# Kernel optimization log

Measured on AMD Instinct MI355X. Metric: run time of the kernel, lower is better.

## Reference

```python
import jax, jax.numpy as jnp
import numpy as np

N_NODES = 50000
N_EDGES = 800000
IN_DIM = 64
HID = 64
NUM_GRAPHS = 512


def _gcn_conv(x, W, b, row, col, norm, n):
    # PyG GCNConv: h = x @ W; out[col] += norm * h[row]; out += b
    h = x @ W  # [N, HID]
    msg = h[row] * norm[:, None]  # [E', HID]
    out = jax.ops.segment_sum(msg, col, num_segments=n)
    return out + b


def setup_inputs() -> dict:
    key = jax.random.key(0)
    ks = jax.random.split(key, 12)
    x = jax.random.normal(ks[0], (N_NODES, IN_DIM), dtype=jnp.float32)
    edge_index = jax.random.randint(ks[1], (2, N_EDGES), 0, N_NODES, dtype=jnp.int64)
    batch = jnp.sort(jax.random.randint(ks[2], (N_NODES,), 0, NUM_GRAPHS, dtype=jnp.int64))
    s = 0.05
    W1 = jax.random.normal(ks[3], (IN_DIM, HID), dtype=jnp.float32) * s
    b1 = jnp.zeros((HID,), dtype=jnp.float32)
    W2 = jax.random.normal(ks[4], (HID, HID), dtype=jnp.float32) * s
    b2 = jnp.zeros((HID,), dtype=jnp.float32)
    W3 = jax.random.normal(ks[5], (HID, HID), dtype=jnp.float32) * s
    b3 = jnp.zeros((HID,), dtype=jnp.float32)
    lin_W = jax.random.normal(ks[6], (HID, 1), dtype=jnp.float32) * s
    lin_b = jnp.zeros((1,), dtype=jnp.float32)
    return {"x": x, "W1": W1, "b1": b1, "W2": W2, "b2": b2, "W3": W3,
            "b3": b3, "lin_W": lin_W, "lin_b": lin_b,
            "edge_index": edge_index, "batch": batch}


def reference(x, W1, b1, W2, b2, W3, b3, lin_W, lin_b, edge_index, batch):
    n = x.shape[0]
    # add self-loops (GCNConv default add_self_loops=True)
    loop = jnp.arange(n, dtype=edge_index.dtype)
    row = jnp.concatenate([edge_index[0], loop])  # source
    col = jnp.concatenate([edge_index[1], loop])  # target (aggregation index)
    # symmetric degree normalization: deg over targets with unit weights
    deg = jax.ops.segment_sum(jnp.ones_like(col, dtype=x.dtype), col, num_segments=n)
    dinv = jnp.where(deg > 0, jax.lax.rsqrt(deg), 0.0)
    norm = dinv[row] * dinv[col]  # [E+N]

    h = jax.nn.relu(_gcn_conv(x, W1, b1, row, col, norm, n))
    h = jax.nn.relu(_gcn_conv(h, W2, b2, row, col, norm, n))
    h = _gcn_conv(h, W3, b3, row, col, norm, n)

    # global_mean_pool over batch ids
    sums = jax.ops.segment_sum(h, batch, num_segments=NUM_GRAPHS)
    cnt = jax.ops.segment_sum(jnp.ones((n,), dtype=h.dtype), batch, num_segments=NUM_GRAPHS)
    pooled = sums / jnp.maximum(cnt, 1.0)[:, None]
    # dropout p=0.5 is identity in eval mode
    return pooled @ lin_W + lin_b  # [NUM_GRAPHS, 1]
```

## Files before the change

### kernel.cpp

```cpp
#include <hip/hip_runtime.h>
#include <hip/hip_fp16.h>

#define NN 50000
#define NE 800000
#define HD 64
#define NG 512
#define NBK 196
#define NBL 196
#define M_CNT (NBK * NBL)
#define NBS 151
#define GEMM_BLOCKS 3125

__global__ void zero_kernel(int* __restrict__ p, int n) {
    int i = blockIdx.x * blockDim.x + threadIdx.x;
    if (i < n) p[i] = 0;
}

__global__ __launch_bounds__(256) void bucket_count(const int* __restrict__ col,
                                                    const int* __restrict__ batch,
                                                    int* __restrict__ counts,
                                                    int* __restrict__ beg,
                                                    int* __restrict__ endx) {
    __shared__ int hist[256];
    int tid = threadIdx.x, blk = blockIdx.x;
    hist[tid] = 0;
    __syncthreads();
    int base = blk * 4096;
#pragma unroll
    for (int k = 0; k < 16; ++k) {
        int e = base + k * 256 + tid;
        if (e < NE) atomicAdd(&hist[col[e] >> 8], 1);
    }
    int t = blk * 256 + tid;
    if (t < NN) {
        int g = batch[t];
        if (t == 0 || batch[t - 1] != g) beg[g] = t;
        if (t == NN - 1 || batch[t + 1] != g) endx[g] = t + 1;
    }
    __syncthreads();
    if (tid < NBK) counts[tid * NBL + blk] = hist[tid];
}

__global__ __launch_bounds__(256) void block_reduce(const int* __restrict__ src,
                                                    int* __restrict__ bsum) {
    __shared__ int ws[4];
    int tid = threadIdx.x, lane = tid & 63, wid = tid >> 6;
    int i = blockIdx.x * 256 + tid;
    int v = (i < M_CNT) ? src[i] : 0;
#pragma unroll
    for (int off = 32; off > 0; off >>= 1) v += __shfl_down(v, off, 64);
    if (lane == 0) ws[wid] = v;
    __syncthreads();
    if (tid == 0) bsum[blockIdx.x] = ws[0] + ws[1] + ws[2] + ws[3];
}

__global__ __launch_bounds__(64) void scan_bsum(int* __restrict__ bsum) {
    int lane = threadIdx.x;
    int carry = 0;
    for (int base = 0; base < NBS; base += 64) {
        int i = base + lane;
        int v = (i < NBS) ? bsum[i] : 0;
        int inc = v;
#pragma unroll
        for (int off = 1; off < 64; off <<= 1) {
            int t = __shfl_up(inc, off, 64);
            if (lane >= off) inc += t;
        }
        if (i < NBS) bsum[i] = carry + inc - v;
        carry += __shfl(inc, 63, 64);
    }
}

__global__ __launch_bounds__(256) void block_scan(const int* __restrict__ src,
                                                  const int* __restrict__ bsum,
                                                  int* __restrict__ dst) {
    __shared__ int ws[4];
    int tid = threadIdx.x, lane = tid & 63, wid = tid >> 6;
    int i = blockIdx.x * 256 + tid;
    int v = (i < M_CNT) ? src[i] : 0;
    int inc = v;
#pragma unroll
    for (int off = 1; off < 64; off <<= 1) {
        int t = __shfl_up(inc, off, 64);
        if (lane >= off) inc += t;
    }
    if (lane == 63) ws[wid] = inc;
    __syncthreads();
    int woff = 0;
    for (int k = 0; k < wid; ++k) woff += ws[k];
    if (i < M_CNT) dst[i] = bsum[blockIdx.x] + woff + inc - v;
}

__global__ __launch_bounds__(256) void gemm1_scatter(const float* __restrict__ x,
                                                     const float* __restrict__ W1,
                                                     __half* __restrict__ h16,
                                                     const int* __restrict__ row,
                                                     const int* __restrict__ col,
                                                     const int* __restrict__ counts_ex,
                                                     unsigned* __restrict__ packed) {
    if (blockIdx.x < GEMM_BLOCKS) {
        __shared__ float Ws[64][64];
        __shared__ float Is[16][64];
        int t = threadIdx.x;
        for (int i = t; i < 64 * 64; i += 256) Ws[i >> 6][i & 63] = W1[i];
        int row0 = blockIdx.x * 16;
        for (int i = t; i < 16 * 64; i += 256)
            Is[i >> 6][i & 63] = x[(row0 + (i >> 6)) * HD + (i & 63)];
        __syncthreads();
        int c = t & 63, r4 = t >> 6;
        float a0 = 0.f, a1 = 0.f, a2 = 0.f, a3 = 0.f;
#pragma unroll
        for (int k = 0; k < 64; ++k) {
            float w = Ws[k][c];
            a0 += Is[r4 + 0][k] * w;
            a1 += Is[r4 + 4][k] * w;
            a2 += Is[r4 + 8][k] * w;
            a3 += Is[r4 + 12][k] * w;
        }
        h16[(row0 + r4 + 0) * HD + c] = __float2half(a0);
        h16[(row0 + r4 + 4) * HD + c] = __float2half(a1);
        h16[(row0 + r4 + 8) * HD + c] = __float2half(a2);
        h16[(row0 + r4 + 12) * HD + c] = __float2half(a3);
    } else {
        __shared__ int cur[256];
        int tid = threadIdx.x, blk = blockIdx.x - GEMM_BLOCKS;
        cur[tid] = 0;
        __syncthreads();
        int base = blk * 4096;
#pragma unroll
        for (int k = 0; k < 16; ++k) {
            int e = base + k * 256 + tid;
            if (e < NE) {
                int c = col[e], r = row[e];
                int b = c >> 8;
                int lpos = atomicAdd(&cur[b], 1);
                int pos = counts_ex[b * NBL + blk] + lpos;
                packed[pos] = (unsigned)r | ((unsigned)(c & 255) << 16);
            }
        }
    }
}

__global__ __launch_bounds__(256) void csr_rowptr(const unsigned* __restrict__ packed,
                                                  const int* __restrict__ counts_ex,
                                                  int* __restrict__ rowptr,
                                                  float* __restrict__ dinv) {
    __shared__ int hist[256];
    __shared__ int ws[4];
    int bkt = blockIdx.x, tid = threadIdx.x;
    int s = counts_ex[bkt * NBL];
    int e = (bkt == NBK - 1) ? NE : counts_ex[(bkt + 1) * NBL];
    hist[tid] = 0;
    __syncthreads();
    for (int j = s + tid; j < e; j += 256)
        atomicAdd(&hist[(packed[j] >> 16) & 255], 1);
    __syncthreads();
    int lane = tid & 63, wid = tid >> 6;
    int v = hist[tid], inc = v;
#pragma unroll
    for (int off = 1; off < 64; off <<= 1) {
        int t = __shfl_up(inc, off, 64);
        if (lane >= off) inc += t;
    }
    if (lane == 63) ws[wid] = inc;
    __syncthreads();
    int woff = 0;
    for (int k = 0; k < wid; ++k) woff += ws[k];
    int node = bkt * 256 + tid;
    if (node < NN) {
        rowptr[node] = s + woff + inc - v;
        dinv[node] = rsqrtf((float)(v + 1));
    }
    if (bkt == 0 && tid == 0) rowptr[NN] = NE;
}

__global__ __launch_bounds__(256) void csr_fill(const unsigned* __restrict__ packed,
                                                const int* __restrict__ counts_ex,
                                                const int* __restrict__ rowptr,
                                                const float* __restrict__ dinv,
                                                int2* __restrict__ ew) {
    __shared__ int cur[256];
    int bkt = blockIdx.x, tid = threadIdx.x;
    int s = counts_ex[bkt * NBL];
    int e = (bkt == NBK - 1) ? NE : counts_ex[(bkt + 1) * NBL];
    cur[tid] = 0;
    __syncthreads();
    for (int j = s + tid; j < e; j += 256) {
        unsigned p = packed[j];
        int r = p & 0xFFFF;
        int lc = (p >> 16) & 255;
        int c = (bkt << 8) | lc;
        int slot = rowptr[c] + atomicAdd(&cur[lc], 1);
        float w = dinv[r] * dinv[c];
        ew[slot] = make_int2(r, __float_as_int(w));
    }
}

__global__ __launch_bounds__(256) void gemm64_f16(const __half* __restrict__ in,
                                                  const float* __restrict__ W,
                                                  __half* __restrict__ out) {
    __shared__ float Ws[64][64];
    __shared__ float Is[16][64];
    int t = threadIdx.x;
    for (int i = t; i < 64 * 64; i += 256) Ws[i >> 6][i & 63] = W[i];
    int row0 = blockIdx.x * 16;
    const __half2* in2 = (const __half2*)(in + (size_t)row0 * HD);
    for (int i = t; i < 16 * 32; i += 256) {
        float2 v = __half22float2(in2[i]);
        int r = i >> 5, c2 = (i & 31) * 2;
        Is[r][c2]     = fmaxf(v.x, 0.f);
        Is[r][c2 + 1] = fmaxf(v.y, 0.f);
    }
    __syncthreads();
    int c = t & 63, r4 = t >> 6;
    float a0 = 0.f, a1 = 0.f, a2 = 0.f, a3 = 0.f;
#pragma unroll
    for (int k = 0; k < 64; ++k) {
        float w = Ws[k][c];
        a0 += Is[r4 + 0][k] * w;
        a1 += Is[r4 + 4][k] * w;
        a2 += Is[r4 + 8][k] * w;
        a3 += Is[r4 + 12][k] * w;
    }
    out[(row0 + r4 + 0) * HD + c] = __float2half(a0);
    out[(row0 + r4 + 4) * HD + c] = __float2half(a1);
    out[(row0 + r4 + 8) * HD + c] = __float2half(a2);
    out[(row0 + r4 + 12) * HD + c] = __float2half(a3);
}

template <bool POOL>
__global__ __launch_bounds__(256) void gather_h16(const __half* __restrict__ h16,
                                                  const int* __restrict__ rowptr,
                                                  const int2* __restrict__ ew,
                                                  const float* __restrict__ dinv,
                                                  const float* __restrict__ b,
                                                  __half* __restrict__ out16,
                                                  const int* __restrict__ batch,
                                                  float* __restrict__ pooled) {
    int tid = threadIdx.x, lane = tid & 63, wid = tid >> 6;
    int hh = lane >> 5, c = lane & 31;
    int node = blockIdx.x * 4 + wid;
    const __half2* hv = (const __half2*)h16;
    int s = rowptr[node], e = rowptr[node + 1];
    float2 acc;
    if (hh == 0) {
        float di = dinv[node], dd = di * di;
        float2 self = __half22float2(hv[node * 32 + c]);
        float2 bb = ((const float2*)b)[c];
        acc.x = dd * self.x + bb.x;
        acc.y = dd * self.y + bb.y;
    } else {
        acc.x = 0.f; acc.y = 0.f;
    }
    int nfull = (e - s) & ~7;
    int j = s + hh, jend = s + nfull;
    for (; j < jend; j += 8) {
        int2 p0 = ew[j], p1 = ew[j + 2], p2 = ew[j + 4], p3 = ew[j + 6];
        __half2 v0 = hv[p0.x * 32 + c];
        __half2 v1 = hv[p1.x * 32 + c];
        __half2 v2 = hv[p2.x * 32 + c];
        __half2 v3 = hv[p3.x * 32 + c];
        float w0 = __int_as_float(p0.y), w1 = __int_as_float(p1.y);
        float w2 = __int_as_float(p2.y), w3 = __int_as_float(p3.y);
        float2 f0 = __half22float2(v0), f1 = __half22float2(v1);
        float2 f2 = __half22float2(v2), f3 = __half22float2(v3);
        acc.x += w0 * f0.x + w1 * f1.x + w2 * f2.x + w3 * f3.x;
        acc.y += w0 * f0.y + w1 * f1.y + w2 * f2.y + w3 * f3.y;
    }
    for (; j < e; j += 2) {
        int2 p = ew[j];
        __half2 v = hv[p.x * 32 + c];
        float w = __int_as_float(p.y);
        float2 f = __half22float2(v);
        acc.x += w * f.x;
        acc.y += w * f.y;
    }
    acc.x += __shfl_xor(acc.x, 32, 64);
    acc.y += __shfl_xor(acc.y, 32, 64);
    if (hh == 0) {
        if (POOL) {
            int g = batch[node];
            atomicAdd(&pooled[g * HD + 2 * c], acc.x);
            atomicAdd(&pooled[g * HD + 2 * c + 1], acc.y);
        } else {
            ((__half2*)out16)[node * 32 + c] = __floats2half2_rn(acc.x, acc.y);
        }
    }
}

__global__ __launch_bounds__(64) void final_kernel(const float* __restrict__ pooled,
                                                   const int* __restrict__ beg,
                                                   const int* __restrict__ endx,
                                                   const float* __restrict__ lin_W,
                                                   const float* __restrict__ lin_b,
                                                   float* __restrict__ out) {
    int g = blockIdx.x, d = threadIdx.x;
    float cnt = (float)(endx[g] - beg[g]);
    float v = pooled[g * HD + d] / fmaxf(cnt, 1.f) * lin_W[d];
#pragma unroll
    for (int off = 32; off > 0; off >>= 1) v += __shfl_down(v, off, 64);
    if (d == 0) out[g] = v + lin_b[0];
}

extern "C" void kernel_launch(void* const* d_in, const int* in_sizes, int n_in,
                              void* d_out, int out_size, void* d_ws, size_t ws_size,
                              hipStream_t stream) {
    const float* x     = (const float*)d_in[0];
    const float* W1    = (const float*)d_in[1];
    const float* b1    = (const float*)d_in[2];
    const float* W2    = (const float*)d_in[3];
    const float* b2    = (const float*)d_in[4];
    const float* W3    = (const float*)d_in[5];
    const float* b3    = (const float*)d_in[6];
    const float* lin_W = (const float*)d_in[7];
    const float* lin_b = (const float*)d_in[8];
    const int* edge_index = (const int*)d_in[9];
    const int* batch      = (const int*)d_in[10];
    const int* row = edge_index;
    const int* col = edge_index + NE;
    float* out = (float*)d_out;

    __half*   h16       = (__half*)d_ws;
    __half*   A16       = h16 + (size_t)NN * HD;
    int2*     ew        = (int2*)(A16 + (size_t)NN * HD);
    unsigned* packed    = (unsigned*)(ew + NE);
    int*      counts    = (int*)(packed + NE);
    int*      counts_ex = counts + M_CNT;
    int*      rowptr    = counts_ex + M_CNT;
    float*    dinv      = (float*)(rowptr + NN + 2);
    int*      bsum      = (int*)(dinv + NN);
    float*    pooled    = (float*)(bsum + 256);
    int*      beg       = (int*)(pooled + NG * HD);
    int*      endx      = beg + NG;

    const int ZN = NG * HD + 2 * NG;
    zero_kernel<<<(ZN + 255) / 256, 256, 0, stream>>>((int*)pooled, ZN);

    bucket_count<<<NBL, 256, 0, stream>>>(col, batch, counts, beg, endx);
    block_reduce<<<NBS, 256, 0, stream>>>(counts, bsum);
    scan_bsum<<<1, 64, 0, stream>>>(bsum);
    block_scan<<<NBS, 256, 0, stream>>>(counts, bsum, counts_ex);
    gemm1_scatter<<<GEMM_BLOCKS + NBL, 256, 0, stream>>>(x, W1, h16, row, col,
                                                         counts_ex, packed);
    csr_rowptr<<<NBK, 256, 0, stream>>>(packed, counts_ex, rowptr, dinv);
    csr_fill<<<NBK, 256, 0, stream>>>(packed, counts_ex, rowptr, dinv, ew);

    const int GB = NN / 4;

    gather_h16<false><<<GB, 256, 0, stream>>>(h16, rowptr, ew, dinv, b1, A16,
                                              batch, pooled);
    gemm64_f16<<<GEMM_BLOCKS, 256, 0, stream>>>(A16, W2, h16);
    gather_h16<false><<<GB, 256, 0, stream>>>(h16, rowptr, ew, dinv, b2, A16,
                                              batch, pooled);
    gemm64_f16<<<GEMM_BLOCKS, 256, 0, stream>>>(A16, W3, h16);
    gather_h16<true><<<GB, 256, 0, stream>>>(h16, rowptr, ew, dinv, b3, nullptr,
                                             batch, pooled);

    final_kernel<<<NG, 64, 0, stream>>>(pooled, beg, endx, lin_W, lin_b, out);
}
```

Baseline: 283.3 us.

## Split feature matrix into two 32-column planes and gather each plane separately

Stores the fp16 hidden features as two planar halves of 32 columns each instead of row-major 64 columns. Each sparse gather pass is now run twice, once per plane, so the gathered working set per pass is half the size and more likely to stay resident in cache. Edge-list reads and output writes switch to nontemporal loads and stores, and each wavefront now covers four edges at a time with 16 lanes. The cost is reading the edge list twice per layer and launching twice as many gather kernels.

```diff
diff --git a/kernel.cpp b/kernel.cpp
--- a/kernel.cpp
+++ b/kernel.cpp
@@ -10,6 +10,7 @@
 #define M_CNT (NBK * NBL)
 #define NBS 151
 #define GEMM_BLOCKS 3125
+
 
 __global__ void zero_kernel(int* __restrict__ p, int n) {
     int i = blockIdx.x * blockDim.x + threadIdx.x;
@@ -117,10 +118,11 @@
             a2 += Is[r4 + 8][k] * w;
             a3 += Is[r4 + 12][k] * w;
         }
-        h16[(row0 + r4 + 0) * HD + c] = __float2half(a0);
-        h16[(row0 + r4 + 4) * HD + c] = __float2half(a1);
-        h16[(row0 + r4 + 8) * HD + c] = __float2half(a2);
-        h16[(row0 + r4 + 12) * HD + c] = __float2half(a3);
+        size_t pb = (size_t)(c >> 5) * NN * 32 + (c & 31);
+        h16[pb + (size_t)(row0 + r4 + 0) * 32] = __float2half(a0);
+        h16[pb + (size_t)(row0 + r4 + 4) * 32] = __float2half(a1);
+        h16[pb + (size_t)(row0 + r4 + 8) * 32] = __float2half(a2);
+        h16[pb + (size_t)(row0 + r4 + 12) * 32] = __float2half(a3);
     } else {
         __shared__ int cur[256];
         int tid = threadIdx.x, blk = blockIdx.x - GEMM_BLOCKS;
@@ -204,12 +206,17 @@
     int t = threadIdx.x;
     for (int i = t; i < 64 * 64; i += 256) Ws[i >> 6][i & 63] = W[i];
     int row0 = blockIdx.x * 16;
-    const __half2* in2 = (const __half2*)(in + (size_t)row0 * HD);
-    for (int i = t; i < 16 * 32; i += 256) {
-        float2 v = __half22float2(in2[i]);
-        int r = i >> 5, c2 = (i & 31) * 2;
-        Is[r][c2]     = fmaxf(v.x, 0.f);
-        Is[r][c2 + 1] = fmaxf(v.y, 0.f);
+    const __half2* p0 = (const __half2*)(in + (size_t)row0 * 32);
+    const __half2* p1 = (const __half2*)(in + ((size_t)NN + row0) * 32);
+    {
+        int i = t;
+        int r = i >> 4, cc = (i & 15) * 2;
+        float2 v = __half22float2(p0[i]);
+        Is[r][cc]     = fmaxf(v.x, 0.f);
+        Is[r][cc + 1] = fmaxf(v.y, 0.f);
+        float2 w = __half22float2(p1[i]);
+        Is[r][32 + cc]     = fmaxf(w.x, 0.f);
+        Is[r][32 + cc + 1] = fmaxf(w.y, 0.f);
     }
     __syncthreads();
     int c = t & 63, r4 = t >> 6;
@@ -222,68 +229,68 @@
         a2 += Is[r4 + 8][k] * w;
         a3 += Is[r4 + 12][k] * w;
     }
-    out[(row0 + r4 + 0) * HD + c] = __float2half(a0);
-    out[(row0 + r4 + 4) * HD + c] = __float2half(a1);
-    out[(row0 + r4 + 8) * HD + c] = __float2half(a2);
-    out[(row0 + r4 + 12) * HD + c] = __float2half(a3);
+    size_t pb = (size_t)(c >> 5) * NN * 32 + (c & 31);
+    out[pb + (size_t)(row0 + r4 + 0) * 32] = __float2half(a0);
+    out[pb + (size_t)(row0 + r4 + 4) * 32] = __float2half(a1);
+    out[pb + (size_t)(row0 + r4 + 8) * 32] = __float2half(a2);
+    out[pb + (size_t)(row0 + r4 + 12) * 32] = __float2half(a3);
 }
 
 template <bool POOL>
-__global__ __launch_bounds__(256) void gather_h16(const __half* __restrict__ h16,
-                                                  const int* __restrict__ rowptr,
-                                                  const int2* __restrict__ ew,
-                                                  const float* __restrict__ dinv,
-                                                  const float* __restrict__ b,
-                                                  __half* __restrict__ out16,
-                                                  const int* __restrict__ batch,
-                                                  float* __restrict__ pooled) {
+__global__ __launch_bounds__(256) void gather_plane(const __half* __restrict__ hp,
+                                                    const int* __restrict__ rowptr,
+                                                    const int2* __restrict__ ew,
+                                                    const float* __restrict__ dinv,
+                                                    const float* __restrict__ bp,
+                                                    __half* __restrict__ outp,
+                                                    const int* __restrict__ batch,
+                                                    float* __restrict__ pooled,
+                                                    int poff) {
     int tid = threadIdx.x, lane = tid & 63, wid = tid >> 6;
-    int hh = lane >> 5, c = lane & 31;
+    int g = lane >> 4, c = lane & 15;
     int node = blockIdx.x * 4 + wid;
-    const __half2* hv = (const __half2*)h16;
+    const __half2* hv = (const __half2*)hp;
     int s = rowptr[node], e = rowptr[node + 1];
-    float2 acc;
-    if (hh == 0) {
+    float2 acc = {0.f, 0.f};
+    if (g == 0) {
         float di = dinv[node], dd = di * di;
-        float2 self = __half22float2(hv[node * 32 + c]);
-        float2 bb = ((const float2*)b)[c];
+        float2 self = __half22float2(hv[node * 16 + c]);
+        float2 bb = ((const float2*)bp)[c];
         acc.x = dd * self.x + bb.x;
         acc.y = dd * self.y + bb.y;
-    } else {
-        acc.x = 0.f; acc.y = 0.f;
-    }
-    int nfull = (e - s) & ~7;
-    int j = s + hh, jend = s + nfull;
-    for (; j < jend; j += 8) {
-        int2 p0 = ew[j], p1 = ew[j + 2], p2 = ew[j + 4], p3 = ew[j + 6];
-        __half2 v0 = hv[p0.x * 32 + c];
-        __half2 v1 = hv[p1.x * 32 + c];
-        __half2 v2 = hv[p2.x * 32 + c];
-        __half2 v3 = hv[p3.x * 32 + c];
-        float w0 = __int_as_float(p0.y), w1 = __int_as_float(p1.y);
-        float w2 = __int_as_float(p2.y), w3 = __int_as_float(p3.y);
-        float2 f0 = __half22float2(v0), f1 = __half22float2(v1);
-        float2 f2 = __half22float2(v2), f3 = __half22float2(v3);
-        acc.x += w0 * f0.x + w1 * f1.x + w2 * f2.x + w3 * f3.x;
-        acc.y += w0 * f0.y + w1 * f1.y + w2 * f2.y + w3 * f3.y;
-    }
-    for (; j < e; j += 2) {
-        int2 p = ew[j];
-        __half2 v = hv[p.x * 32 + c];
-        float w = __int_as_float(p.y);
-        float2 f = __half22float2(v);
+    }
+    int j = s + g;
+    for (; j + 4 < e; j += 8) {
+        long long q0 = __builtin_nontemporal_load((const long long*)(ew + j));
+        long long q1 = __builtin_nontemporal_load((const long long*)(ew + j + 4));
+        int s0 = (int)q0, s1 = (int)q1;
+        float w0 = __int_as_float((int)(q0 >> 32));
+        float w1 = __int_as_float((int)(q1 >> 32));
+        float2 f0 = __half22float2(hv[s0 * 16 + c]);
+        float2 f1 = __half22float2(hv[s1 * 16 + c]);
+        acc.x += w0 * f0.x + w1 * f1.x;
+        acc.y += w0 * f0.y + w1 * f1.y;
+    }
+    if (j < e) {
+        long long q = __builtin_nontemporal_load((const long long*)(ew + j));
+        float w = __int_as_float((int)(q >> 32));
+        float2 f = __half22float2(hv[((int)q) * 16 + c]);
         acc.x += w * f.x;
         acc.y += w * f.y;
     }
+    acc.x += __shfl_xor(acc.x, 16, 64);
+    acc.y += __shfl_xor(acc.y, 16, 64);
     acc.x += __shfl_xor(acc.x, 32, 64);
     acc.y += __shfl_xor(acc.y, 32, 64);
-    if (hh == 0) {
+    if (g == 0) {
         if (POOL) {
-            int g = batch[node];
-            atomicAdd(&pooled[g * HD + 2 * c], acc.x);
-            atomicAdd(&pooled[g * HD + 2 * c + 1], acc.y);
+            int gr = batch[node];
+            atomicAdd(&pooled[gr * HD + poff + 2 * c], acc.x);
+            atomicAdd(&pooled[gr * HD + poff + 2 * c + 1], acc.y);
         } else {
-            ((__half2*)out16)[node * 32 + c] = __floats2half2_rn(acc.x, acc.y);
+            union { __half2 h; unsigned u; } cv;
+            cv.h = __floats2half2_rn(acc.x, acc.y);
+            __builtin_nontemporal_store(cv.u, (unsigned*)outp + node * 16 + c);
         }
     }
 }
@@ -333,6 +340,8 @@
     int*      beg       = (int*)(pooled + NG * HD);
     int*      endx      = beg + NG;
 
+    const size_t PL = (size_t)NN * 32;
+
     const int ZN = NG * HD + 2 * NG;
     zero_kernel<<<(ZN + 255) / 256, 256, 0, stream>>>((int*)pooled, ZN);
 
@@ -347,14 +356,20 @@
 
     const int GB = NN / 4;
 
-    gather_h16<false><<<GB, 256, 0, stream>>>(h16, rowptr, ew, dinv, b1, A16,
-                                              batch, pooled);
+    gather_plane<false><<<GB, 256, 0, stream>>>(h16, rowptr, ew, dinv, b1, A16,
+                                                batch, pooled, 0);
+    gather_plane<false><<<GB, 256, 0, stream>>>(h16 + PL, rowptr, ew, dinv,
+                                                b1 + 32, A16 + PL, batch, pooled, 32);
     gemm64_f16<<<GEMM_BLOCKS, 256, 0, stream>>>(A16, W2, h16);
-    gather_h16<false><<<GB, 256, 0, stream>>>(h16, rowptr, ew, dinv, b2, A16,
-                                              batch, pooled);
+    gather_plane<false><<<GB, 256, 0, stream>>>(h16, rowptr, ew, dinv, b2, A16,
+                                                batch, pooled, 0);
+    gather_plane<false><<<GB, 256, 0, stream>>>(h16 + PL, rowptr, ew, dinv,
+                                                b2 + 32, A16 + PL, batch, pooled, 32);
     gemm64_f16<<<GEMM_BLOCKS, 256, 0, stream>>>(A16, W3, h16);
-    gather_h16<true><<<GB, 256, 0, stream>>>(h16, rowptr, ew, dinv, b3, nullptr,
-                                             batch, pooled);
+    gather_plane<true><<<GB, 256, 0, stream>>>(h16, rowptr, ew, dinv, b3, nullptr,
+                                               batch, pooled, 0);
+    gather_plane<true><<<GB, 256, 0, stream>>>(h16 + PL, rowptr, ew, dinv,
+                                               b3 + 32, nullptr, batch, pooled, 32);
 
     final_kernel<<<NG, 64, 0, stream>>>(pooled, beg, endx, lin_W, lin_b, out);
 }
```

Result: slower. 350.1 us (+23.6%).

## Store only edge sources in CSR and compute normalization weights on the fly

Applied to the files above, without the earlier changes.

The CSR fill now writes only a 4-byte source index per edge instead of an int2 holding source and precomputed weight. The gather kernel loads 64 edge indices per wave in one coalesced read, looks up dinv per source, and broadcasts both via shuffles. It factors the target's dinv out of the sum and applies it once at the end. This halves edge-list traffic in each of the three gather passes, at the cost of an extra dinv gather per edge, more shuffles, and a padded tail that loads masked-out rows.

```diff
diff --git a/kernel.cpp b/kernel.cpp
--- a/kernel.cpp
+++ b/kernel.cpp
@@ -10,6 +10,7 @@
 #define M_CNT (NBK * NBL)
 #define NBS 151
 #define GEMM_BLOCKS 3125
+
 
 __global__ void zero_kernel(int* __restrict__ p, int n) {
     int i = blockIdx.x * blockDim.x + threadIdx.x;
@@ -177,8 +178,7 @@
 __global__ __launch_bounds__(256) void csr_fill(const unsigned* __restrict__ packed,
                                                 const int* __restrict__ counts_ex,
                                                 const int* __restrict__ rowptr,
-                                                const float* __restrict__ dinv,
-                                                int2* __restrict__ ew) {
+                                                int* __restrict__ esrc) {
     __shared__ int cur[256];
     int bkt = blockIdx.x, tid = threadIdx.x;
     int s = counts_ex[bkt * NBL];
@@ -187,12 +187,9 @@
     __syncthreads();
     for (int j = s + tid; j < e; j += 256) {
         unsigned p = packed[j];
-        int r = p & 0xFFFF;
         int lc = (p >> 16) & 255;
-        int c = (bkt << 8) | lc;
-        int slot = rowptr[c] + atomicAdd(&cur[lc], 1);
-        float w = dinv[r] * dinv[c];
-        ew[slot] = make_int2(r, __float_as_int(w));
+        int slot = rowptr[(bkt << 8) | lc] + atomicAdd(&cur[lc], 1);
+        esrc[slot] = (int)(p & 0xFFFF);
     }
 }
 
@@ -229,61 +226,69 @@
 }
 
 template <bool POOL>
-__global__ __launch_bounds__(256) void gather_h16(const __half* __restrict__ h16,
-                                                  const int* __restrict__ rowptr,
-                                                  const int2* __restrict__ ew,
-                                                  const float* __restrict__ dinv,
-                                                  const float* __restrict__ b,
-                                                  __half* __restrict__ out16,
-                                                  const int* __restrict__ batch,
-                                                  float* __restrict__ pooled) {
+__global__ __launch_bounds__(256) void gather_s(const __half* __restrict__ hp,
+                                                const int* __restrict__ rowptr,
+                                                const int* __restrict__ esrc,
+                                                const float* __restrict__ dinv,
+                                                const float* __restrict__ b,
+                                                __half* __restrict__ out16,
+                                                const int* __restrict__ batch,
+                                                float* __restrict__ pooled) {
     int tid = threadIdx.x, lane = tid & 63, wid = tid >> 6;
     int hh = lane >> 5, c = lane & 31;
     int node = blockIdx.x * 4 + wid;
-    const __half2* hv = (const __half2*)h16;
+    const __half2* hv = (const __half2*)hp;
     int s = rowptr[node], e = rowptr[node + 1];
-    float2 acc;
-    if (hh == 0) {
-        float di = dinv[node], dd = di * di;
-        float2 self = __half22float2(hv[node * 32 + c]);
-        float2 bb = ((const float2*)b)[c];
-        acc.x = dd * self.x + bb.x;
-        acc.y = dd * self.y + bb.y;
-    } else {
-        acc.x = 0.f; acc.y = 0.f;
-    }
-    int nfull = (e - s) & ~7;
-    int j = s + hh, jend = s + nfull;
-    for (; j < jend; j += 8) {
-        int2 p0 = ew[j], p1 = ew[j + 2], p2 = ew[j + 4], p3 = ew[j + 6];
-        __half2 v0 = hv[p0.x * 32 + c];
-        __half2 v1 = hv[p1.x * 32 + c];
-        __half2 v2 = hv[p2.x * 32 + c];
-        __half2 v3 = hv[p3.x * 32 + c];
-        float w0 = __int_as_float(p0.y), w1 = __int_as_float(p1.y);
-        float w2 = __int_as_float(p2.y), w3 = __int_as_float(p3.y);
-        float2 f0 = __half22float2(v0), f1 = __half22float2(v1);
-        float2 f2 = __half22float2(v2), f3 = __half22float2(v3);
-        acc.x += w0 * f0.x + w1 * f1.x + w2 * f2.x + w3 * f3.x;
-        acc.y += w0 * f0.y + w1 * f1.y + w2 * f2.y + w3 * f3.y;
-    }
-    for (; j < e; j += 2) {
-        int2 p = ew[j];
-        __half2 v = hv[p.x * 32 + c];
-        float w = __int_as_float(p.y);
-        float2 f = __half22float2(v);
-        acc.x += w * f.x;
-        acc.y += w * f.y;
+    int deg = e - s;
+    float2 acc = {0.f, 0.f};
+    for (int k = 0; k < deg; k += 64) {
+        int my = esrc[s + k + lane] & 0xFFFF;
+        float myw = dinv[my];
+        int nk = min(deg - k, 64);
+        int nmain = nk >> 3;
+        for (int j = 0; j < nmain; ++j) {
+            int t = j * 8 + hh;
+            int s0 = __shfl(my, t, 64);
+            int s1 = __shfl(my, t + 2, 64);
+            int s2 = __shfl(my, t + 4, 64);
+            int s3 = __shfl(my, t + 6, 64);
+            float w0 = __shfl(myw, t, 64);
+            float w1 = __shfl(myw, t + 2, 64);
+            float w2 = __shfl(myw, t + 4, 64);
+            float w3 = __shfl(myw, t + 6, 64);
+            float2 f0 = __half22float2(hv[s0 * 32 + c]);
+            float2 f1 = __half22float2(hv[s1 * 32 + c]);
+            float2 f2 = __half22float2(hv[s2 * 32 + c]);
+            float2 f3 = __half22float2(hv[s3 * 32 + c]);
+            acc.x += w0 * f0.x + w1 * f1.x + w2 * f2.x + w3 * f3.x;
+            acc.y += w0 * f0.y + w1 * f1.y + w2 * f2.y + w3 * f3.y;
+        }
+        int tbase = (nk & ~7) + hh;
+#pragma unroll
+        for (int u = 0; u < 4; ++u) {
+            int t = tbase + 2 * u;
+            int sl = __shfl(my, t & 63, 64);
+            float w = __shfl(myw, t & 63, 64);
+            float wm = (t < nk) ? w : 0.f;
+            float2 f = __half22float2(hv[sl * 32 + c]);
+            acc.x += wm * f.x;
+            acc.y += wm * f.y;
+        }
     }
     acc.x += __shfl_xor(acc.x, 32, 64);
     acc.y += __shfl_xor(acc.y, 32, 64);
     if (hh == 0) {
+        float di = dinv[node];
+        float2 self = __half22float2(hv[node * 32 + c]);
+        float2 bb = ((const float2*)b)[c];
+        float vx = di * acc.x + di * di * self.x + bb.x;
+        float vy = di * acc.y + di * di * self.y + bb.y;
         if (POOL) {
             int g = batch[node];
-            atomicAdd(&pooled[g * HD + 2 * c], acc.x);
-            atomicAdd(&pooled[g * HD + 2 * c + 1], acc.y);
+            atomicAdd(&pooled[g * HD + 2 * c], vx);
+            atomicAdd(&pooled[g * HD + 2 * c + 1], vy);
         } else {
-            ((__half2*)out16)[node * 32 + c] = __floats2half2_rn(acc.x, acc.y);
+            ((__half2*)out16)[node * 32 + c] = __floats2half2_rn(vx, vy);
         }
     }
 }
@@ -322,8 +327,8 @@
 
     __half*   h16       = (__half*)d_ws;
     __half*   A16       = h16 + (size_t)NN * HD;
-    int2*     ew        = (int2*)(A16 + (size_t)NN * HD);
-    unsigned* packed    = (unsigned*)(ew + NE);
+    int*      esrc      = (int*)(A16 + (size_t)NN * HD);
+    unsigned* packed    = (unsigned*)(esrc + NE + 64);
     int*      counts    = (int*)(packed + NE);
     int*      counts_ex = counts + M_CNT;
     int*      rowptr    = counts_ex + M_CNT;
@@ -335,6 +340,7 @@
 
     const int ZN = NG * HD + 2 * NG;
     zero_kernel<<<(ZN + 255) / 256, 256, 0, stream>>>((int*)pooled, ZN);
+    zero_kernel<<<1, 64, 0, stream>>>(esrc + NE, 64);
 
     bucket_count<<<NBL, 256, 0, stream>>>(col, batch, counts, beg, endx);
     block_reduce<<<NBS, 256, 0, stream>>>(counts, bsum);
@@ -343,18 +349,18 @@
     gemm1_scatter<<<GEMM_BLOCKS + NBL, 256, 0, stream>>>(x, W1, h16, row, col,
                                                          counts_ex, packed);
     csr_rowptr<<<NBK, 256, 0, stream>>>(packed, counts_ex, rowptr, dinv);
-    csr_fill<<<NBK, 256, 0, stream>>>(packed, counts_ex, rowptr, dinv, ew);
+    csr_fill<<<NBK, 256, 0, stream>>>(packed, counts_ex, rowptr, esrc);
 
     const int GB = NN / 4;
 
-    gather_h16<false><<<GB, 256, 0, stream>>>(h16, rowptr, ew, dinv, b1, A16,
-                                              batch, pooled);
+    gather_s<false><<<GB, 256, 0, stream>>>(h16, rowptr, esrc, dinv, b1, A16,
+                                            batch, pooled);
     gemm64_f16<<<GEMM_BLOCKS, 256, 0, stream>>>(A16, W2, h16);
-    gather_h16<false><<<GB, 256, 0, stream>>>(h16, rowptr, ew, dinv, b2, A16,
-                                              batch, pooled);
+    gather_s<false><<<GB, 256, 0, stream>>>(h16, rowptr, esrc, dinv, b2, A16,
+                                            batch, pooled);
     gemm64_f16<<<GEMM_BLOCKS, 256, 0, stream>>>(A16, W3, h16);
-    gather_h16<true><<<GB, 256, 0, stream>>>(h16, rowptr, ew, dinv, b3, nullptr,
-                                             batch, pooled);
+    gather_s<true><<<GB, 256, 0, stream>>>(h16, rowptr, esrc, dinv, b3, nullptr,
+                                           batch, pooled);
 
     final_kernel<<<NG, 64, 0, stream>>>(pooled, beg, endx, lin_W, lin_b, out);
 }
```

Measured after the change: 271.3 us. 1.04x faster.
